# Kernel optimization log

Hardware: AMD Instinct MI355X
Metric: run time of the kernel (lower is better)

Reference implementation:

```python
import jax, jax.numpy as jnp
import numpy as np

HEADS = 2
C1 = 33    # per-head out channels, conv1
C2 = 550   # per-head out channels, conv2


def _lin_params(key, fan_in, fan_out):
    kw, kb = jax.random.split(key)
    scale = 1.0 / np.sqrt(fan_in)
    W = jax.random.uniform(kw, (fan_in, fan_out), jnp.float32, -scale, scale)
    b = jax.random.uniform(kb, (fan_out,), jnp.float32, -scale, scale)
    return W, b


def transformer_conv(x, src, dst, Wq, bq, Wk, bk, Wv, bv, Ws, bs, heads, out_ch):
    """PyG TransformerConv (concat=True, root_weight=True, beta=False)."""
    N = x.shape[0]
    q = (x @ Wq + bq).reshape(N, heads, out_ch)  # query of target node i
    k = (x @ Wk + bk).reshape(N, heads, out_ch)  # key of source node j
    v = (x @ Wv + bv).reshape(N, heads, out_ch)  # value of source node j
    # attention logits per edge: [E, H]
    alpha = jnp.einsum('ehc,ehc->eh', q[dst], k[src]) / jnp.sqrt(jnp.float32(out_ch))
    # segment softmax over incoming edges of each dst node
    m = jax.lax.stop_gradient(jax.ops.segment_max(alpha, dst, num_segments=N))  # [N,H]
    e = jnp.exp(alpha - m[dst])
    denom = jax.ops.segment_sum(e, dst, num_segments=N)  # [N,H]
    a = e / denom[dst]
    # weighted scatter-aggregate of source values: [N,H,C]
    out = jax.ops.segment_sum(a[..., None] * v[src], dst, num_segments=N)
    out = out.reshape(N, heads * out_ch)
    # root/skip connection
    out = out + x @ Ws + bs
    return out


def setup_inputs() -> dict:
    key = jax.random.key(0)
    ks = jax.random.split(key, 10)
    N, E, IN = 20000, 120000, 256
    x = jax.random.normal(ks[0], (N, IN), jnp.float32)
    edge_index = jax.random.randint(ks[1], (2, E), 0, N, jnp.int64 if jax.config.jax_enable_x64 else jnp.int32)
    d = {'x': x, 'edge_index': edge_index}
    # conv1: IN -> heads*C1
    d['Wq1'], d['bq1'] = _lin_params(ks[2], IN, HEADS * C1)
    d['Wk1'], d['bk1'] = _lin_params(ks[3], IN, HEADS * C1)
    d['Wv1'], d['bv1'] = _lin_params(ks[4], IN, HEADS * C1)
    d['Ws1'], d['bs1'] = _lin_params(ks[5], IN, HEADS * C1)
    # conv2: heads*C1 -> heads*C2
    IN2 = HEADS * C1
    d['Wq2'], d['bq2'] = _lin_params(ks[6], IN2, HEADS * C2)
    d['Wk2'], d['bk2'] = _lin_params(ks[7], IN2, HEADS * C2)
    d['Wv2'], d['bv2'] = _lin_params(ks[8], IN2, HEADS * C2)
    d['Ws2'], d['bs2'] = _lin_params(ks[9], IN2, HEADS * C2)
    return d


def reference(x, edge_index, Wq1, bq1, Wk1, bk1, Wv1, bv1, Ws1, bs1,
              Wq2, bq2, Wk2, bk2, Wv2, bv2, Ws2, bs2):
    src, dst = edge_index[0], edge_index[1]
    h = transformer_conv(x, src, dst, Wq1, bq1, Wk1, bk1, Wv1, bv1, Ws1, bs1, HEADS, C1)
    h = transformer_conv(h, src, dst, Wq2, bq2, Wk2, bk2, Wv2, bv2, Ws2, bs2, HEADS, C2)
    # x.view(N, 550, heads).max(dim=2) -- faithful to the original reshape layout
    h = h.reshape(h.shape[0], C2, HEADS)
    return jnp.max(h, axis=2)
```

## Files before the change

### kernel.cpp

```cpp
#include <hip/hip_runtime.h>
#include <math.h>

#define HEADS 2
#define C1    33
#define C2    550
#define D1    66
#define D2    1100
#define IN1   256
#define PROJW 288
#define KU    224
#define N2P   1152
#define KZ    96
#define ZW    144

typedef __attribute__((ext_vector_type(8))) short bfrag;
typedef __attribute__((ext_vector_type(4))) float f32x4;

__device__ inline unsigned short f2bf(float f) {
    unsigned int u = __float_as_uint(f);
    u += 0x7FFFu + ((u >> 16) & 1u);
    return (unsigned short)(u >> 16);
}

__device__ inline int xcd_slot(int bid, int slots) {
    return (bid >> 3) + (bid & 7) * slots;
}

__global__ void k_cvt(const float* __restrict__ x, unsigned short* __restrict__ xb, int total4) {
    int i = blockIdx.x * blockDim.x + threadIdx.x;
    if (i >= total4) return;
    float4 v = ((const float4*)x)[i];
    ushort4 o;
    o.x = f2bf(v.x); o.y = f2bf(v.y); o.z = f2bf(v.z); o.w = f2bf(v.w);
    ((ushort4*)xb)[i] = o;
}

__global__ void k_prep1(const float* __restrict__ Wq, const float* __restrict__ bq,
                        const float* __restrict__ Wk, const float* __restrict__ bk,
                        const float* __restrict__ Wv, const float* __restrict__ bv,
                        const float* __restrict__ Ws, const float* __restrict__ bs,
                        unsigned short* __restrict__ Wt1, float* __restrict__ bcat) {
    int bid = blockIdx.x;
    int lk = bid & 3, t = bid >> 2;
    int ks = t & 7, g = t >> 3;
    int col = threadIdx.x;
    int c = g * 96 + col;
    int k0 = ks * 32 + lk * 8;
    short vals[8];
    float bia = 0.f;
    if (c < 4 * D1) {
        int m = c / D1, j = c % D1;
        const float* W; const float* B;
        switch (m) {
            case 0: W = Wq; B = bq; break;
            case 1: W = Wk; B = bk; break;
            case 2: W = Wv; B = bv; break;
            default: W = Ws; B = bs; break;
        }
        #pragma unroll
        for (int e = 0; e < 8; e++) vals[e] = (short)f2bf(W[(size_t)(k0 + e) * D1 + j]);
        bia = B[j];
    } else {
        #pragma unroll
        for (int e = 0; e < 8; e++) vals[e] = 0;
    }
    *(bfrag*)&Wt1[((size_t)bid * 96 + col) * 8] = *(bfrag*)vals;
    if (ks == 0 && lk == 0) bcat[c] = bia;
}

__global__ void k_prep2(const float* __restrict__ Wv2, const float* __restrict__ bv2,
                        const float* __restrict__ Ws2, const float* __restrict__ bs2,
                        unsigned short* __restrict__ W2t) {
    int bid = blockIdx.x;
    int lk = bid & 3, t = bid >> 2;
    int ks = t % 7, g = t / 7;
    int col = threadIdx.x;
    int c = g * 96 + col;
    int k0 = ks * 32 + lk * 8;
    short vals[8];
    #pragma unroll
    for (int e = 0; e < 8; e++) {
        int k = k0 + e;
        float val = 0.f;
        if (c < D2) {
            if (c < C2) {
                if (k < 66) val = Wv2[(size_t)k * D2 + c];
                else if (k >= 132 && k < 198) val = Ws2[(size_t)(k - 132) * D2 + c];
                else if (k == 198) val = bv2[c];
                else if (k == 223) val = bs2[c];
            } else {
                if (k >= 66 && k < 132) val = Wv2[(size_t)(k - 66) * D2 + c];
                else if (k >= 132 && k < 198) val = Ws2[(size_t)(k - 132) * D2 + c];
                else if (k == 199) val = bv2[c];
                else if (k == 223) val = bs2[c];
            }
        }
        vals[e] = (short)f2bf(val);
    }
    *(bfrag*)&W2t[((size_t)bid * 96 + col) * 8] = *(bfrag*)vals;
}

__global__ void k_hist(const int* __restrict__ dst, int E, int* __restrict__ cnt) {
    int e = blockIdx.x * blockDim.x + threadIdx.x;
    if (e < E) atomicAdd(&cnt[dst[e]], 1);
}

__global__ void k_scan(const int* __restrict__ cnt, int* __restrict__ roff,
                       int* __restrict__ pos, int N) {
    __shared__ int wsum[16];
    __shared__ int carry_s;
    int tid = threadIdx.x, wid = tid >> 6, lane = tid & 63;
    if (tid == 0) { carry_s = 0; roff[0] = 0; }
    __syncthreads();
    for (int base = 0; base < N; base += 1024) {
        int i = base + tid;
        int v = (i < N) ? cnt[i] : 0;
        int x = v;
        #pragma unroll
        for (int s = 1; s < 64; s <<= 1) {
            int t = __shfl_up(x, s, 64);
            if (lane >= s) x += t;
        }
        if (lane == 63) wsum[wid] = x;
        __syncthreads();
        if (tid < 16) {
            int y = wsum[tid];
            #pragma unroll
            for (int s = 1; s < 16; s <<= 1) {
                int t = __shfl_up(y, s, 16);
                if (tid >= s) y += t;
            }
            wsum[tid] = y;
        }
        __syncthreads();
        int carry = carry_s;
        int incl = carry + (wid ? wsum[wid - 1] : 0) + x;
        if (i < N) { roff[i + 1] = incl; pos[i] = incl - v; }
        __syncthreads();
        if (tid == 0) carry_s = carry + wsum[15];
        __syncthreads();
    }
}

__global__ void k_fill(const int* __restrict__ src, const int* __restrict__ dst, int E,
                       int* __restrict__ pos, int* __restrict__ elist) {
    int e = blockIdx.x * blockDim.x + threadIdx.x;
    if (e < E) {
        int slot = atomicAdd(&pos[dst[e]], 1);
        elist[slot] = src[e];
    }
}

__global__ __launch_bounds__(256) void k_mm1(
        const unsigned short* __restrict__ A, const unsigned short* __restrict__ B,
        const float* __restrict__ bias, float* __restrict__ proj, int N,
        int nRow, int slots) {
    int s = xcd_slot(blockIdx.x, slots);
    if (s >= nRow * 3) return;
    int rowt = s / 3, g = s - rowt * 3;
    int cbase = g * 96;
    int wave = threadIdx.x >> 6, lane = threadIdx.x & 63;
    int lr = lane & 15, lk = lane >> 4;
    int rbase = rowt * 128 + wave * 32;
    int ar[2];
    #pragma unroll
    for (int mi = 0; mi < 2; mi++) {
        int r = rbase + mi * 16 + lr;
        ar[mi] = (r < N) ? r : (N - 1);
    }
    bfrag a[2][8];
    #pragma unroll
    for (int mi = 0; mi < 2; mi++)
        #pragma unroll
        for (int ks = 0; ks < 8; ks++)
            a[mi][ks] = *(const bfrag*)(A + (size_t)ar[mi] * IN1 + ks * 32 + lk * 8);
    f32x4 acc[2][6];
    #pragma unroll
    for (int mi = 0; mi < 2; mi++)
        #pragma unroll
        for (int ni = 0; ni < 6; ni++) acc[mi][ni] = (f32x4){0.f, 0.f, 0.f, 0.f};
    #pragma unroll
    for (int ks = 0; ks < 8; ks++) {
        bfrag b[6];
        #pragma unroll
        for (int ni = 0; ni < 6; ni++)
            b[ni] = *(const bfrag*)(B + (size_t)(g * 8 + ks) * 3072 + lk * 768 + (ni * 16 + lr) * 8);
        #pragma unroll
        for (int mi = 0; mi < 2; mi++)
            #pragma unroll
            for (int ni = 0; ni < 6; ni++)
                acc[mi][ni] = __builtin_amdgcn_mfma_f32_16x16x32_bf16(a[mi][ks], b[ni], acc[mi][ni], 0, 0, 0);
    }
    #pragma unroll
    for (int mi = 0; mi < 2; mi++) {
        #pragma unroll
        for (int ni = 0; ni < 6; ni++) {
            int col = cbase + ni * 16 + lr;
            float bia = bias[col];
            #pragma unroll
            for (int r = 0; r < 4; r++) {
                int row = rbase + mi * 16 + lk * 4 + r;
                if (row < N) proj[(size_t)row * PROJW + col] = acc[mi][ni][r] + bia;
            }
        }
    }
}

__global__ __launch_bounds__(128) void k_conv1(
        const float* __restrict__ proj, const int* __restrict__ roff,
        const int* __restrict__ elist, float* __restrict__ h1,
        unsigned short* __restrict__ h1b, int N) {
    int n = blockIdx.x;
    int h = threadIdx.x >> 6;
    int lane = threadIdx.x & 63;
    size_t pb = (size_t)n * PROJW;
    int hc = h * C1;
    bool ok = (lane < C1);
    float my_q = ok ? proj[pb + hc + lane] : 0.f;
    float s1v  = ok ? proj[pb + 198 + hc + lane] : 0.f;
    float m = -INFINITY, lsum = 0.f, acc = 0.f;
    int e0 = roff[n], e1 = roff[n + 1];
    const float isc = 0.17407765595569785f;
    int e = e0;
    for (; e + 3 < e1; e += 4) {
        int s0 = elist[e], s1 = elist[e + 1], s2 = elist[e + 2], s3 = elist[e + 3];
        size_t b0 = (size_t)s0 * PROJW, b1 = (size_t)s1 * PROJW;
        size_t b2 = (size_t)s2 * PROJW, b3 = (size_t)s3 * PROJW;
        float k0 = ok ? proj[b0 + 66 + hc + lane] : 0.f;
        float k1 = ok ? proj[b1 + 66 + hc + lane] : 0.f;
        float k2 = ok ? proj[b2 + 66 + hc + lane] : 0.f;
        float k3 = ok ? proj[b3 + 66 + hc + lane] : 0.f;
        float v0 = ok ? proj[b0 + 132 + hc + lane] : 0.f;
        float v1 = ok ? proj[b1 + 132 + hc + lane] : 0.f;
        float v2 = ok ? proj[b2 + 132 + hc + lane] : 0.f;
        float v3 = ok ? proj[b3 + 132 + hc + lane] : 0.f;
        float p0 = my_q * k0, p1 = my_q * k1, p2 = my_q * k2, p3 = my_q * k3;
        #pragma unroll
        for (int off = 32; off >= 1; off >>= 1) {
            p0 += __shfl_xor(p0, off, 64);
            p1 += __shfl_xor(p1, off, 64);
            p2 += __shfl_xor(p2, off, 64);
            p3 += __shfl_xor(p3, off, 64);
        }
        float a0 = p0 * isc, a1 = p1 * isc, a2 = p2 * isc, a3 = p3 * isc;
        float mp = fmaxf(fmaxf(a0, a1), fmaxf(a2, a3));
        float e0v = __expf(a0 - mp), e1v = __expf(a1 - mp);
        float e2v = __expf(a2 - mp), e3v = __expf(a3 - mp);
        float lp = (e0v + e1v) + (e2v + e3v);
        float ap = (e0v * v0 + e1v * v1) + (e2v * v2 + e3v * v3);
        float mnew = fmaxf(m, mp);
        float sc = __expf(m - mnew), sp = __expf(mp - mnew);
        lsum = lsum * sc + lp * sp;
        acc  = acc * sc + ap * sp;
        m = mnew;
    }
    for (; e + 1 < e1; e += 2) {
        int sa = elist[e], sb = elist[e + 1];
        size_t ba = (size_t)sa * PROJW, bb = (size_t)sb * PROJW;
        float ka = ok ? proj[ba + 66 + hc + lane] : 0.f;
        float va = ok ? proj[ba + 132 + hc + lane] : 0.f;
        float kb = ok ? proj[bb + 66 + hc + lane] : 0.f;
        float vb = ok ? proj[bb + 132 + hc + lane] : 0.f;
        float pa = my_q * ka, pbv = my_q * kb;
        #pragma unroll
        for (int off = 32; off >= 1; off >>= 1) {
            pa  += __shfl_xor(pa, off, 64);
            pbv += __shfl_xor(pbv, off, 64);
        }
        float aa = pa * isc, ab = pbv * isc;
        float mp = fmaxf(aa, ab);
        float ea = __expf(aa - mp), eb = __expf(ab - mp);
        float lp = ea + eb, ap = ea * va + eb * vb;
        float mnew = fmaxf(m, mp);
        float sc = __expf(m - mnew), sp = __expf(mp - mnew);
        lsum = lsum * sc + lp * sp;
        acc  = acc * sc + ap * sp;
        m = mnew;
    }
    if (e < e1) {
        int s = elist[e];
        size_t sb = (size_t)s * PROJW;
        float kv = ok ? proj[sb + 66 + hc + lane] : 0.f;
        float vv = ok ? proj[sb + 132 + hc + lane] : 0.f;
        float prod = my_q * kv;
        #pragma unroll
        for (int off = 32; off >= 1; off >>= 1) prod += __shfl_xor(prod, off, 64);
        float alpha = prod * isc;
        float mnew = fmaxf(m, alpha);
        float sc = __expf(m - mnew);
        float p = __expf(alpha - mnew);
        lsum = lsum * sc + p;
        acc  = acc * sc + p * vv;
        m = mnew;
    }
    if (ok) {
        float res = (lsum > 0.f) ? acc / lsum : 0.f;
        float val = res + s1v;
        h1[(size_t)n * D1 + hc + lane] = val;
        h1b[(size_t)n * KZ + hc + lane] = f2bf(val);
    } else if (h == 1 && lane >= C1 && lane < C1 + 30) {
        h1b[(size_t)n * KZ + D1 + (lane - C1)] = 0;
    }
}

__global__ __launch_bounds__(256) void k_precomp(
        const float* __restrict__ Wq2, const float* __restrict__ bq2,
        const float* __restrict__ Wk2, const float* __restrict__ bk2,
        float* __restrict__ G, float* __restrict__ wqbk,
        float* __restrict__ wkbq, float* __restrict__ cc) {
    int wave = threadIdx.x >> 6, lane = threadIdx.x & 63;
    int j = blockIdx.x * 4 + wave;
    if (j >= 8978) return;
    const float *u, *v;
    float* outp;
    if (j < 8976) {
        int h = j / 4488;
        int r = j % 4488;
        int a = r / 68, b = r % 68;
        if (b < 66)      { u = Wq2 + (size_t)a * D2 + h * C2; v = Wk2 + (size_t)b * D2 + h * C2; outp = &G[h * 4356 + a * 66 + b]; }
        else if (b == 66){ u = Wq2 + (size_t)a * D2 + h * C2; v = bk2 + h * C2;                  outp = &wqbk[h * 66 + a]; }
        else             { u = Wk2 + (size_t)a * D2 + h * C2; v = bq2 + h * C2;                  outp = &wkbq[h * 66 + a]; }
    } else {
        int h = j - 8976;
        u = bq2 + h * C2; v = bk2 + h * C2; outp = &cc[h];
    }
    float acc = 0.f;
    for (int c = lane; c < C2; c += 64) acc += u[c] * v[c];
    #pragma unroll
    for (int off = 32; off >= 1; off >>= 1) acc += __shfl_xor(acc, off, 64);
    if (lane == 0) *outp = acc;
}

__global__ void k_prepz(const float* __restrict__ G, const float* __restrict__ wqbk,
                        const float* __restrict__ wkbq, unsigned short* __restrict__ GBt) {
    int bid = blockIdx.x;
    int lk = bid & 3, t = bid >> 2;
    int ks = t % 3, g = t / 3;
    int col = threadIdx.x;
    int r = g * 96 + col;
    int k0 = ks * 32 + lk * 8;
    short vals[8];
    #pragma unroll
    for (int e = 0; e < 8; e++) {
        int k = k0 + e;
        float v = 0.f;
        if (k < D1) {
            if (r < 132) v = G[r * D1 + k];
            else if (r < 134) v = wqbk[(r - 132) * D1 + k];
            else if (r < 136) v = wkbq[(r - 134) * D1 + k];
        }
        vals[e] = (short)f2bf(v);
    }
    *(bfrag*)&GBt[((size_t)bid * 96 + col) * 8] = *(bfrag*)vals;
}

__global__ __launch_bounds__(256) void k_mmz(
        const unsigned short* __restrict__ A, const unsigned short* __restrict__ B,
        float* __restrict__ Z, int N, int nRow, int slots) {
    int s = xcd_slot(blockIdx.x, slots);
    if (s >= nRow * 2) return;
    int rowt = s >> 1, g = s & 1;
    int wave = threadIdx.x >> 6, lane = threadIdx.x & 63;
    int lr = lane & 15, lk = lane >> 4;
    int rbase = rowt * 64 + (wave >> 1) * 32;
    int ch = (wave & 1) * 48;
    int cbase = g * 96 + ch;
    f32x4 acc[2][3];
    #pragma unroll
    for (int i = 0; i < 2; i++)
        #pragma unroll
        for (int j = 0; j < 3; j++) acc[i][j] = (f32x4){0.f, 0.f, 0.f, 0.f};
    int ar[2];
    #pragma unroll
    for (int mi = 0; mi < 2; mi++) {
        int r = rbase + mi * 16 + lr;
        ar[mi] = (r < N) ? r : (N - 1);
    }
    #pragma unroll
    for (int ks = 0; ks < 3; ks++) {
        bfrag a[2], b[3];
        #pragma unroll
        for (int mi = 0; mi < 2; mi++)
            a[mi] = *(const bfrag*)(A + (size_t)ar[mi] * KZ + ks * 32 + lk * 8);
        #pragma unroll
        for (int ni = 0; ni < 3; ni++)
            b[ni] = *(const bfrag*)(B + (size_t)(g * 3 + ks) * 3072 + lk * 768 + (ch + ni * 16 + lr) * 8);
        #pragma unroll
        for (int mi = 0; mi < 2; mi++)
            #pragma unroll
            for (int ni = 0; ni < 3; ni++)
                acc[mi][ni] = __builtin_amdgcn_mfma_f32_16x16x32_bf16(a[mi], b[ni], acc[mi][ni], 0, 0, 0);
    }
    #pragma unroll
    for (int mi = 0; mi < 2; mi++) {
        #pragma unroll
        for (int ni = 0; ni < 3; ni++) {
            int col = cbase + ni * 16 + lr;
            if (col >= 136) continue;
            #pragma unroll
            for (int r = 0; r < 4; r++) {
                int row = rbase + mi * 16 + lk * 4 + r;
                if (row < N) Z[(size_t)row * ZW + col] = acc[mi][ni][r];
            }
        }
    }
}

__global__ __launch_bounds__(128) void k_conv2(
        const float* __restrict__ h1, const float* __restrict__ Z,
        const float* __restrict__ cc, const int* __restrict__ roff,
        const int* __restrict__ elist, unsigned short* __restrict__ U, int N) {
    int n = blockIdx.x;
    int h = threadIdx.x >> 6;
    int lane = threadIdx.x & 63;
    int c0 = lane, c1 = lane + 64;
    bool ok1 = (c1 < D1);
    float hd0 = h1[(size_t)n * D1 + c0];
    float hd1 = ok1 ? h1[(size_t)n * D1 + c1] : 0.f;
    float adv = Z[(size_t)n * ZW + 132 + h] + cc[h];
    float m = -INFINITY, lsum = 0.f, a0 = 0.f, a1 = 0.f;
    int e0 = roff[n], e1 = roff[n + 1];
    const float isc = 0.04264014327112209f;
    int hD = h * D1;
    int e = e0;
    for (; e + 3 < e1; e += 4) {
        int s0 = elist[e], s1 = elist[e + 1], s2 = elist[e + 2], s3 = elist[e + 3];
        const float* z0 = Z + (size_t)s0 * ZW;
        const float* z1 = Z + (size_t)s1 * ZW;
        const float* z2 = Z + (size_t)s2 * ZW;
        const float* z3 = Z + (size_t)s3 * ZW;
        float p0 = hd0 * z0[hD + c0] + (ok1 ? hd1 * z0[hD + c1] : 0.f);
        float p1 = hd0 * z1[hD + c0] + (ok1 ? hd1 * z1[hD + c1] : 0.f);
        float p2 = hd0 * z2[hD + c0] + (ok1 ? hd1 * z2[hD + c1] : 0.f);
        float p3 = hd0 * z3[hD + c0] + (ok1 ? hd1 * z3[hD + c1] : 0.f);
        #pragma unroll
        for (int off = 32; off >= 1; off >>= 1) {
            p0 += __shfl_xor(p0, off, 64);
            p1 += __shfl_xor(p1, off, 64);
            p2 += __shfl_xor(p2, off, 64);
            p3 += __shfl_xor(p3, off, 64);
        }
        float al0 = (p0 + adv + z0[134 + h]) * isc;
        float al1 = (p1 + adv + z1[134 + h]) * isc;
        float al2 = (p2 + adv + z2[134 + h]) * isc;
        float al3 = (p3 + adv + z3[134 + h]) * isc;
        float va00 = h1[(size_t)s0 * D1 + c0];
        float va01 = ok1 ? h1[(size_t)s0 * D1 + c1] : 0.f;
        float va10 = h1[(size_t)s1 * D1 + c0];
        float va11 = ok1 ? h1[(size_t)s1 * D1 + c1] : 0.f;
        float va20 = h1[(size_t)s2 * D1 + c0];
        float va21 = ok1 ? h1[(size_t)s2 * D1 + c1] : 0.f;
        float va30 = h1[(size_t)s3 * D1 + c0];
        float va31 = ok1 ? h1[(size_t)s3 * D1 + c1] : 0.f;
        float mp = fmaxf(fmaxf(al0, al1), fmaxf(al2, al3));
        float e0v = __expf(al0 - mp), e1v = __expf(al1 - mp);
        float e2v = __expf(al2 - mp), e3v = __expf(al3 - mp);
        float lp = (e0v + e1v) + (e2v + e3v);
        float ap0 = (e0v * va00 + e1v * va10) + (e2v * va20 + e3v * va30);
        float ap1 = (e0v * va01 + e1v * va11) + (e2v * va21 + e3v * va31);
        float mnew = fmaxf(m, mp);
        float sc = __expf(m - mnew), sp = __expf(mp - mnew);
        lsum = lsum * sc + lp * sp;
        a0 = a0 * sc + ap0 * sp;
        a1 = a1 * sc + ap1 * sp;
        m = mnew;
    }
    for (; e + 1 < e1; e += 2) {
        int sa = elist[e], sb = elist[e + 1];
        const float* za = Z + (size_t)sa * ZW;
        const float* zb = Z + (size_t)sb * ZW;
        float pa = hd0 * za[hD + c0] + (ok1 ? hd1 * za[hD + c1] : 0.f);
        float pb = hd0 * zb[hD + c0] + (ok1 ? hd1 * zb[hD + c1] : 0.f);
        #pragma unroll
        for (int off = 32; off >= 1; off >>= 1) {
            pa += __shfl_xor(pa, off, 64);
            pb += __shfl_xor(pb, off, 64);
        }
        float aa = (pa + adv + za[134 + h]) * isc;
        float ab = (pb + adv + zb[134 + h]) * isc;
        float va0 = h1[(size_t)sa * D1 + c0];
        float va1 = ok1 ? h1[(size_t)sa * D1 + c1] : 0.f;
        float vb0 = h1[(size_t)sb * D1 + c0];
        float vb1 = ok1 ? h1[(size_t)sb * D1 + c1] : 0.f;
        float mp = fmaxf(aa, ab);
        float ea = __expf(aa - mp), eb = __expf(ab - mp);
        float lp = ea + eb;
        float ap0 = ea * va0 + eb * vb0;
        float ap1 = ea * va1 + eb * vb1;
        float mnew = fmaxf(m, mp);
        float sc = __expf(m - mnew), sp = __expf(mp - mnew);
        lsum = lsum * sc + lp * sp;
        a0 = a0 * sc + ap0 * sp;
        a1 = a1 * sc + ap1 * sp;
        m = mnew;
    }
    if (e < e1) {
        int s = elist[e];
        const float* zr = Z + (size_t)s * ZW;
        float prod = hd0 * zr[hD + c0] + (ok1 ? hd1 * zr[hD + c1] : 0.f);
        #pragma unroll
        for (int off = 32; off >= 1; off >>= 1) prod += __shfl_xor(prod, off, 64);
        float alpha = (prod + adv + zr[134 + h]) * isc;
        float mnew = fmaxf(m, alpha);
        float sc = __expf(m - mnew);
        float p = __expf(alpha - mnew);
        lsum = lsum * sc + p;
        float v0 = h1[(size_t)s * D1 + c0];
        float vv1 = ok1 ? h1[(size_t)s * D1 + c1] : 0.f;
        a0 = a0 * sc + p * v0;
        a1 = a1 * sc + p * vv1;
        m = mnew;
    }
    float inv = (lsum > 0.f) ? 1.f / lsum : 0.f;
    size_t ub = (size_t)n * KU;
    U[ub + hD + c0] = f2bf(a0 * inv);
    if (ok1) U[ub + hD + c1] = f2bf(a1 * inv);
    if (lane == 0) U[ub + 198 + h] = (lsum > 0.f) ? (unsigned short)0x3F80 : (unsigned short)0;
    if (h == 0) {
        U[ub + 132 + c0] = f2bf(hd0);
        if (ok1) U[ub + 132 + c1] = f2bf(hd1);
        if (lane == 1) U[ub + 223] = (unsigned short)0x3F80;
    } else if (lane >= 34 && lane < 57) {
        U[ub + 200 + (lane - 34)] = 0;
    }
}

__global__ __launch_bounds__(256) void k_mm2(
        const unsigned short* __restrict__ A, const unsigned short* __restrict__ B,
        float* __restrict__ out, int N, int nRow, int slots) {
    __shared__ float ot[4][32][49];
    int s = xcd_slot(blockIdx.x, slots);
    if (s >= nRow * 12) return;
    int rowt = s / 12, g = s - rowt * 12;
    int wave = threadIdx.x >> 6, lane = threadIdx.x & 63;
    int lr = lane & 15, lk = lane >> 4;
    int rbase = rowt * 128 + wave * 32;
    int ar[2];
    #pragma unroll
    for (int mi = 0; mi < 2; mi++) {
        int r = rbase + mi * 16 + lr;
        ar[mi] = (r < N) ? r : (N - 1);
    }
    bfrag a[2][7];
    #pragma unroll
    for (int mi = 0; mi < 2; mi++)
        #pragma unroll
        for (int ks = 0; ks < 7; ks++)
            a[mi][ks] = *(const bfrag*)(A + (size_t)ar[mi] * KU + ks * 32 + lk * 8);
    f32x4 acc[2][6];
    #pragma unroll
    for (int mi = 0; mi < 2; mi++)
        #pragma unroll
        for (int ni = 0; ni < 6; ni++) acc[mi][ni] = (f32x4){0.f, 0.f, 0.f, 0.f};
    #pragma unroll
    for (int ks = 0; ks < 7; ks++) {
        bfrag b[6];
        #pragma unroll
        for (int ni = 0; ni < 6; ni++)
            b[ni] = *(const bfrag*)(B + (size_t)(g * 7 + ks) * 3072 + lk * 768 + (ni * 16 + lr) * 8);
        #pragma unroll
        for (int mi = 0; mi < 2; mi++)
            #pragma unroll
            for (int ni = 0; ni < 6; ni++)
                acc[mi][ni] = __builtin_amdgcn_mfma_f32_16x16x32_bf16(a[mi][ks], b[ni], acc[mi][ni], 0, 0, 0);
    }
    #pragma unroll
    for (int mi = 0; mi < 2; mi++) {
        #pragma unroll
        for (int ni = 0; ni < 6; ni++) {
            #pragma unroll
            for (int r = 0; r < 4; r++) {
                float val = acc[mi][ni][r];
                float oth = __shfl_xor(val, 1, 64);
                if (!(lane & 1))
                    ot[wave][mi * 16 + lk * 4 + r][ni * 8 + (lr >> 1)] = fmaxf(val, oth);
            }
        }
    }
    __syncthreads();
    int colb = g * 48;
    #pragma unroll
    for (int i = 0; i < 24; i++) {
        int t = i * 64 + lane;
        int r32 = t / 48, pos = t - r32 * 48;
        int row = rbase + r32;
        int col = colb + pos;
        if (row < N && col < C2)
            out[(size_t)row * C2 + col] = ot[wave][r32][pos];
    }
}

extern "C" void kernel_launch(void* const* d_in, const int* in_sizes, int n_in,
                              void* d_out, int out_size, void* d_ws, size_t ws_size,
                              hipStream_t stream) {
    const float* x  = (const float*)d_in[0];
    const int*   ei = (const int*)d_in[1];
    int N = in_sizes[0] / IN1;
    int E = in_sizes[1] / 2;
    const int* src = ei;
    const int* dst = ei + E;

    const float *Wq1 = (const float*)d_in[2],  *bq1 = (const float*)d_in[3];
    const float *Wk1 = (const float*)d_in[4],  *bk1 = (const float*)d_in[5];
    const float *Wv1 = (const float*)d_in[6],  *bv1 = (const float*)d_in[7];
    const float *Ws1 = (const float*)d_in[8],  *bs1 = (const float*)d_in[9];
    const float *Wq2 = (const float*)d_in[10], *bq2 = (const float*)d_in[11];
    const float *Wk2 = (const float*)d_in[12], *bk2 = (const float*)d_in[13];
    const float *Wv2 = (const float*)d_in[14], *bv2 = (const float*)d_in[15];
    const float *Ws2 = (const float*)d_in[16], *bs2 = (const float*)d_in[17];

    char* w = (char*)d_ws;
    size_t off = 0;
    auto take = [&](size_t bytes) { size_t o = off; off = (off + bytes + 255) & ~(size_t)255; return o; };

    unsigned short* xb = (unsigned short*)(w + take((size_t)N * IN1 * 2));
    size_t proj_off = take((size_t)N * PROJW * 4);
    float* proj = (float*)(w + proj_off);
    float* Z = proj;
    unsigned short* U = (unsigned short*)(w + proj_off + (size_t)N * ZW * 4);
    float* h1   = (float*)(w + take((size_t)N * D1 * 4));
    unsigned short* h1b = (unsigned short*)(w + take((size_t)N * KZ * 2));
    float* G    = (float*)(w + take((size_t)2 * D1 * D1 * 4));
    float* wqbk = (float*)(w + take(2 * D1 * 4));
    float* wkbq = (float*)(w + take(2 * D1 * 4));
    float* cc   = (float*)(w + take(2 * 4));
    unsigned short* GBt = (unsigned short*)(w + take((size_t)24 * 96 * 8 * 2));
    unsigned short* Wt1 = (unsigned short*)(w + take((size_t)96 * 96 * 8 * 2));
    float* bcat = (float*)(w + take(PROJW * 4));
    unsigned short* W2t = (unsigned short*)(w + take((size_t)336 * 96 * 8 * 2));
    int* cnt   = (int*)(w + take((size_t)N * 4));
    int* roff  = (int*)(w + take((size_t)(N + 1) * 4));
    int* pos   = (int*)(w + take((size_t)N * 4));
    int* elist = (int*)(w + take((size_t)E * 4));

    hipMemsetAsync(cnt, 0, (size_t)N * sizeof(int), stream);
    k_hist<<<(E + 255) / 256, 256, 0, stream>>>(dst, E, cnt);
    k_scan<<<1, 1024, 0, stream>>>(cnt, roff, pos, N);
    k_fill<<<(E + 255) / 256, 256, 0, stream>>>(src, dst, E, pos, elist);

    k_cvt<<<(N * IN1 / 4 + 255) / 256, 256, 0, stream>>>(x, xb, N * IN1 / 4);
    k_prep1<<<96, 96, 0, stream>>>(Wq1, bq1, Wk1, bk1, Wv1, bv1, Ws1, bs1, Wt1, bcat);
    k_prep2<<<336, 96, 0, stream>>>(Wv2, bv2, Ws2, bs2, W2t);
    k_precomp<<<(8978 + 3) / 4, 256, 0, stream>>>(Wq2, bq2, Wk2, bk2, G, wqbk, wkbq, cc);
    k_prepz<<<24, 96, 0, stream>>>(G, wqbk, wkbq, GBt);

    int nRow1 = (N + 127) / 128;
    int tot1  = nRow1 * 3;
    int slots1 = (tot1 + 7) / 8;
    int nRowZ = (N + 63) / 64;
    int totZ  = nRowZ * 2;
    int slotsZ = (totZ + 7) / 8;
    int nRow2 = (N + 127) / 128;
    int tot2  = nRow2 * 12;
    int slots2 = (tot2 + 7) / 8;

    k_mm1<<<slots1 * 8, 256, 0, stream>>>(xb, Wt1, bcat, proj, N, nRow1, slots1);
    k_conv1<<<N, 128, 0, stream>>>(proj, roff, elist, h1, h1b, N);

    k_mmz<<<slotsZ * 8, 256, 0, stream>>>(h1b, GBt, Z, N, nRowZ, slotsZ);

    k_conv2<<<N, 128, 0, stream>>>(h1, Z, cc, roff, elist, U, N);

    k_mm2<<<slots2 * 8, 256, 0, stream>>>(U, W2t, (float*)d_out, N, nRow2, slots2);
}
```

Measured before the change: 174.8 us.

## Split each wave into two half-waves processing alternate edges in graph attention kernels

Both edge-aggregation kernels (conv1 and conv2) now give each 32-lane half of a wavefront alternating edges. Each half handles its feature slice with 32-wide lane coverage and reduces dot products with 5-step 32-lane shuffles instead of 6-step 64-lane ones. At the end the two halves' online-softmax partial states (max, sum, accumulators) are merged with cross-half shuffles. This is meant to use idle lanes (33 of 64 were active in conv1) and to halve per-edge shuffle latency. In exchange it adds a few extra predicated loads and a final merge step.

```diff
diff --git a/kernel.cpp b/kernel.cpp
--- a/kernel.cpp
+++ b/kernel.cpp
@@ -213,93 +213,89 @@
     int n = blockIdx.x;
     int h = threadIdx.x >> 6;
     int lane = threadIdx.x & 63;
+    int half = lane >> 5, l32 = lane & 31;
     size_t pb = (size_t)n * PROJW;
     int hc = h * C1;
-    bool ok = (lane < C1);
-    float my_q = ok ? proj[pb + hc + lane] : 0.f;
-    float s1v  = ok ? proj[pb + 198 + hc + lane] : 0.f;
-    float m = -INFINITY, lsum = 0.f, acc = 0.f;
-    int e0 = roff[n], e1 = roff[n + 1];
+    float q_a = proj[pb + hc + l32];
+    float q_b = (l32 == 0) ? proj[pb + hc + 32] : 0.f;
+    int E0 = roff[n], E1 = roff[n + 1];
+    float m = -INFINITY, lsum = 0.f, aca = 0.f, acb = 0.f;
     const float isc = 0.17407765595569785f;
-    int e = e0;
-    for (; e + 3 < e1; e += 4) {
-        int s0 = elist[e], s1 = elist[e + 1], s2 = elist[e + 2], s3 = elist[e + 3];
+    int i = E0 + half;
+    for (; i + 2 < E1; i += 4) {
+        int s0 = elist[i], s1 = elist[i + 2];
         size_t b0 = (size_t)s0 * PROJW, b1 = (size_t)s1 * PROJW;
-        size_t b2 = (size_t)s2 * PROJW, b3 = (size_t)s3 * PROJW;
-        float k0 = ok ? proj[b0 + 66 + hc + lane] : 0.f;
-        float k1 = ok ? proj[b1 + 66 + hc + lane] : 0.f;
-        float k2 = ok ? proj[b2 + 66 + hc + lane] : 0.f;
-        float k3 = ok ? proj[b3 + 66 + hc + lane] : 0.f;
-        float v0 = ok ? proj[b0 + 132 + hc + lane] : 0.f;
-        float v1 = ok ? proj[b1 + 132 + hc + lane] : 0.f;
-        float v2 = ok ? proj[b2 + 132 + hc + lane] : 0.f;
-        float v3 = ok ? proj[b3 + 132 + hc + lane] : 0.f;
-        float p0 = my_q * k0, p1 = my_q * k1, p2 = my_q * k2, p3 = my_q * k3;
-        #pragma unroll
-        for (int off = 32; off >= 1; off >>= 1) {
-            p0 += __shfl_xor(p0, off, 64);
-            p1 += __shfl_xor(p1, off, 64);
-            p2 += __shfl_xor(p2, off, 64);
-            p3 += __shfl_xor(p3, off, 64);
-        }
-        float a0 = p0 * isc, a1 = p1 * isc, a2 = p2 * isc, a3 = p3 * isc;
-        float mp = fmaxf(fmaxf(a0, a1), fmaxf(a2, a3));
-        float e0v = __expf(a0 - mp), e1v = __expf(a1 - mp);
-        float e2v = __expf(a2 - mp), e3v = __expf(a3 - mp);
-        float lp = (e0v + e1v) + (e2v + e3v);
-        float ap = (e0v * v0 + e1v * v1) + (e2v * v2 + e3v * v3);
+        float k0a = proj[b0 + 66 + hc + l32];
+        float k0b = (l32 == 0) ? proj[b0 + 66 + hc + 32] : 0.f;
+        float k1a = proj[b1 + 66 + hc + l32];
+        float k1b = (l32 == 0) ? proj[b1 + 66 + hc + 32] : 0.f;
+        float v0a = proj[b0 + 132 + hc + l32];
+        float v0b = (l32 == 0) ? proj[b0 + 132 + hc + 32] : 0.f;
+        float v1a = proj[b1 + 132 + hc + l32];
+        float v1b = (l32 == 0) ? proj[b1 + 132 + hc + 32] : 0.f;
+        float p0 = q_a * k0a + q_b * k0b;
+        float p1 = q_a * k1a + q_b * k1b;
+        #pragma unroll
+        for (int off = 16; off >= 1; off >>= 1) {
+            p0 += __shfl_xor(p0, off, 32);
+            p1 += __shfl_xor(p1, off, 32);
+        }
+        float a0 = p0 * isc, a1 = p1 * isc;
+        float mp = fmaxf(a0, a1);
+        float e0 = __expf(a0 - mp), e1 = __expf(a1 - mp);
+        float lp = e0 + e1;
+        float apa = e0 * v0a + e1 * v1a;
+        float apb = e0 * v0b + e1 * v1b;
         float mnew = fmaxf(m, mp);
         float sc = __expf(m - mnew), sp = __expf(mp - mnew);
         lsum = lsum * sc + lp * sp;
-        acc  = acc * sc + ap * sp;
+        aca = aca * sc + apa * sp;
+        acb = acb * sc + apb * sp;
         m = mnew;
     }
-    for (; e + 1 < e1; e += 2) {
-        int sa = elist[e], sb = elist[e + 1];
-        size_t ba = (size_t)sa * PROJW, bb = (size_t)sb * PROJW;
-        float ka = ok ? proj[ba + 66 + hc + lane] : 0.f;
-        float va = ok ? proj[ba + 132 + hc + lane] : 0.f;
-        float kb = ok ? proj[bb + 66 + hc + lane] : 0.f;
-        float vb = ok ? proj[bb + 132 + hc + lane] : 0.f;
-        float pa = my_q * ka, pbv = my_q * kb;
-        #pragma unroll
-        for (int off = 32; off >= 1; off >>= 1) {
-            pa  += __shfl_xor(pa, off, 64);
-            pbv += __shfl_xor(pbv, off, 64);
-        }
-        float aa = pa * isc, ab = pbv * isc;
-        float mp = fmaxf(aa, ab);
-        float ea = __expf(aa - mp), eb = __expf(ab - mp);
-        float lp = ea + eb, ap = ea * va + eb * vb;
-        float mnew = fmaxf(m, mp);
-        float sc = __expf(m - mnew), sp = __expf(mp - mnew);
-        lsum = lsum * sc + lp * sp;
-        acc  = acc * sc + ap * sp;
-        m = mnew;
-    }
-    if (e < e1) {
-        int s = elist[e];
+    for (; i < E1; i += 2) {
+        int s = elist[i];
         size_t sb = (size_t)s * PROJW;
-        float kv = ok ? proj[sb + 66 + hc + lane] : 0.f;
-        float vv = ok ? proj[sb + 132 + hc + lane] : 0.f;
-        float prod = my_q * kv;
-        #pragma unroll
-        for (int off = 32; off >= 1; off >>= 1) prod += __shfl_xor(prod, off, 64);
-        float alpha = prod * isc;
+        float ka = proj[sb + 66 + hc + l32];
+        float kb = (l32 == 0) ? proj[sb + 66 + hc + 32] : 0.f;
+        float va = proj[sb + 132 + hc + l32];
+        float vb = (l32 == 0) ? proj[sb + 132 + hc + 32] : 0.f;
+        float p = q_a * ka + q_b * kb;
+        #pragma unroll
+        for (int off = 16; off >= 1; off >>= 1) p += __shfl_xor(p, off, 32);
+        float alpha = p * isc;
         float mnew = fmaxf(m, alpha);
         float sc = __expf(m - mnew);
-        float p = __expf(alpha - mnew);
-        lsum = lsum * sc + p;
-        acc  = acc * sc + p * vv;
+        float pe = __expf(alpha - mnew);
+        lsum = lsum * sc + pe;
+        aca = aca * sc + pe * va;
+        acb = acb * sc + pe * vb;
         m = mnew;
     }
-    if (ok) {
-        float res = (lsum > 0.f) ? acc / lsum : 0.f;
-        float val = res + s1v;
-        h1[(size_t)n * D1 + hc + lane] = val;
-        h1b[(size_t)n * KZ + hc + lane] = f2bf(val);
-    } else if (h == 1 && lane >= C1 && lane < C1 + 30) {
-        h1b[(size_t)n * KZ + D1 + (lane - C1)] = 0;
+    float mO  = __shfl_xor(m, 32, 64);
+    float lO  = __shfl_xor(lsum, 32, 64);
+    float aaO = __shfl_xor(aca, 32, 64);
+    float abO = __shfl_xor(acb, 32, 64);
+    float mnew = fmaxf(m, mO);
+    float sS = (m  > -INFINITY) ? __expf(m  - mnew) : 0.f;
+    float sO = (mO > -INFINITY) ? __expf(mO - mnew) : 0.f;
+    lsum = lsum * sS + lO * sO;
+    aca  = aca * sS + aaO * sO;
+    acb  = acb * sS + abO * sO;
+    float inv = (lsum > 0.f) ? 1.f / lsum : 0.f;
+    if (half == 0) {
+        float s1a = proj[pb + 198 + hc + l32];
+        float val = aca * inv + s1a;
+        h1[(size_t)n * D1 + hc + l32] = val;
+        h1b[(size_t)n * KZ + hc + l32] = f2bf(val);
+        if (l32 == 0) {
+            float s1b = proj[pb + 198 + hc + 32];
+            float valb = acb * inv + s1b;
+            h1[(size_t)n * D1 + hc + 32] = valb;
+            h1b[(size_t)n * KZ + hc + 32] = f2bf(valb);
+        }
+    } else if (h == 1 && l32 < 30) {
+        h1b[(size_t)n * KZ + D1 + l32] = 0;
     }
 }
 
@@ -413,115 +409,101 @@
     int n = blockIdx.x;
     int h = threadIdx.x >> 6;
     int lane = threadIdx.x & 63;
-    int c0 = lane, c1 = lane + 64;
-    bool ok1 = (c1 < D1);
-    float hd0 = h1[(size_t)n * D1 + c0];
-    float hd1 = ok1 ? h1[(size_t)n * D1 + c1] : 0.f;
+    int half = lane >> 5, l32 = lane & 31;
+    int hD = h * D1;
+    size_t nb = (size_t)n * D1;
+    float hd_a = h1[nb + l32];
+    float hd_b = h1[nb + 32 + l32];
+    float hd_c = (l32 < 2) ? h1[nb + 64 + l32] : 0.f;
     float adv = Z[(size_t)n * ZW + 132 + h] + cc[h];
-    float m = -INFINITY, lsum = 0.f, a0 = 0.f, a1 = 0.f;
-    int e0 = roff[n], e1 = roff[n + 1];
+    int E0 = roff[n], E1 = roff[n + 1];
+    float m = -INFINITY, lsum = 0.f, aa = 0.f, ab = 0.f, ac = 0.f;
     const float isc = 0.04264014327112209f;
-    int hD = h * D1;
-    int e = e0;
-    for (; e + 3 < e1; e += 4) {
-        int s0 = elist[e], s1 = elist[e + 1], s2 = elist[e + 2], s3 = elist[e + 3];
+    int i = E0 + half;
+    for (; i + 2 < E1; i += 4) {
+        int s0 = elist[i], s1 = elist[i + 2];
         const float* z0 = Z + (size_t)s0 * ZW;
         const float* z1 = Z + (size_t)s1 * ZW;
-        const float* z2 = Z + (size_t)s2 * ZW;
-        const float* z3 = Z + (size_t)s3 * ZW;
-        float p0 = hd0 * z0[hD + c0] + (ok1 ? hd1 * z0[hD + c1] : 0.f);
-        float p1 = hd0 * z1[hD + c0] + (ok1 ? hd1 * z1[hD + c1] : 0.f);
-        float p2 = hd0 * z2[hD + c0] + (ok1 ? hd1 * z2[hD + c1] : 0.f);
-        float p3 = hd0 * z3[hD + c0] + (ok1 ? hd1 * z3[hD + c1] : 0.f);
-        #pragma unroll
-        for (int off = 32; off >= 1; off >>= 1) {
-            p0 += __shfl_xor(p0, off, 64);
-            p1 += __shfl_xor(p1, off, 64);
-            p2 += __shfl_xor(p2, off, 64);
-            p3 += __shfl_xor(p3, off, 64);
-        }
-        float al0 = (p0 + adv + z0[134 + h]) * isc;
-        float al1 = (p1 + adv + z1[134 + h]) * isc;
-        float al2 = (p2 + adv + z2[134 + h]) * isc;
-        float al3 = (p3 + adv + z3[134 + h]) * isc;
-        float va00 = h1[(size_t)s0 * D1 + c0];
-        float va01 = ok1 ? h1[(size_t)s0 * D1 + c1] : 0.f;
-        float va10 = h1[(size_t)s1 * D1 + c0];
-        float va11 = ok1 ? h1[(size_t)s1 * D1 + c1] : 0.f;
-        float va20 = h1[(size_t)s2 * D1 + c0];
-        float va21 = ok1 ? h1[(size_t)s2 * D1 + c1] : 0.f;
-        float va30 = h1[(size_t)s3 * D1 + c0];
-        float va31 = ok1 ? h1[(size_t)s3 * D1 + c1] : 0.f;
-        float mp = fmaxf(fmaxf(al0, al1), fmaxf(al2, al3));
-        float e0v = __expf(al0 - mp), e1v = __expf(al1 - mp);
-        float e2v = __expf(al2 - mp), e3v = __expf(al3 - mp);
-        float lp = (e0v + e1v) + (e2v + e3v);
-        float ap0 = (e0v * va00 + e1v * va10) + (e2v * va20 + e3v * va30);
-        float ap1 = (e0v * va01 + e1v * va11) + (e2v * va21 + e3v * va31);
+        float z0c = (l32 < 2) ? z0[hD + 64 + l32] : 0.f;
+        float z1c = (l32 < 2) ? z1[hD + 64 + l32] : 0.f;
+        float p0 = hd_a * z0[hD + l32] + hd_b * z0[hD + 32 + l32] + hd_c * z0c;
+        float p1 = hd_a * z1[hD + l32] + hd_b * z1[hD + 32 + l32] + hd_c * z1c;
+        float as0 = z0[134 + h], as1 = z1[134 + h];
+        #pragma unroll
+        for (int off = 16; off >= 1; off >>= 1) {
+            p0 += __shfl_xor(p0, off, 32);
+            p1 += __shfl_xor(p1, off, 32);
+        }
+        float al0 = (p0 + adv + as0) * isc;
+        float al1 = (p1 + adv + as1) * isc;
+        size_t v0b = (size_t)s0 * D1, v1b = (size_t)s1 * D1;
+        float v0a = h1[v0b + l32], v0bb = h1[v0b + 32 + l32];
+        float v0c = (l32 < 2) ? h1[v0b + 64 + l32] : 0.f;
+        float v1a = h1[v1b + l32], v1bb = h1[v1b + 32 + l32];
+        float v1c = (l32 < 2) ? h1[v1b + 64 + l32] : 0.f;
+        float mp = fmaxf(al0, al1);
+        float e0 = __expf(al0 - mp), e1 = __expf(al1 - mp);
+        float lp = e0 + e1;
         float mnew = fmaxf(m, mp);
         float sc = __expf(m - mnew), sp = __expf(mp - mnew);
         lsum = lsum * sc + lp * sp;
-        a0 = a0 * sc + ap0 * sp;
-        a1 = a1 * sc + ap1 * sp;
+        aa = aa * sc + (e0 * v0a + e1 * v1a) * sp;
+        ab = ab * sc + (e0 * v0bb + e1 * v1bb) * sp;
+        ac = ac * sc + (e0 * v0c + e1 * v1c) * sp;
         m = mnew;
     }
-    for (; e + 1 < e1; e += 2) {
-        int sa = elist[e], sb = elist[e + 1];
-        const float* za = Z + (size_t)sa * ZW;
-        const float* zb = Z + (size_t)sb * ZW;
-        float pa = hd0 * za[hD + c0] + (ok1 ? hd1 * za[hD + c1] : 0.f);
-        float pb = hd0 * zb[hD + c0] + (ok1 ? hd1 * zb[hD + c1] : 0.f);
-        #pragma unroll
-        for (int off = 32; off >= 1; off >>= 1) {
-            pa += __shfl_xor(pa, off, 64);
-            pb += __shfl_xor(pb, off, 64);
-        }
-        float aa = (pa + adv + za[134 + h]) * isc;
-        float ab = (pb + adv + zb[134 + h]) * isc;
-        float va0 = h1[(size_t)sa * D1 + c0];
-        float va1 = ok1 ? h1[(size_t)sa * D1 + c1] : 0.f;
-        float vb0 = h1[(size_t)sb * D1 + c0];
-        float vb1 = ok1 ? h1[(size_t)sb * D1 + c1] : 0.f;
-        float mp = fmaxf(aa, ab);
-        float ea = __expf(aa - mp), eb = __expf(ab - mp);
-        float lp = ea + eb;
-        float ap0 = ea * va0 + eb * vb0;
-        float ap1 = ea * va1 + eb * vb1;
-        float mnew = fmaxf(m, mp);
-        float sc = __expf(m - mnew), sp = __expf(mp - mnew);
-        lsum = lsum * sc + lp * sp;
-        a0 = a0 * sc + ap0 * sp;
-        a1 = a1 * sc + ap1 * sp;
-        m = mnew;
-    }
-    if (e < e1) {
-        int s = elist[e];
+    for (; i < E1; i += 2) {
+        int s = elist[i];
         const float* zr = Z + (size_t)s * ZW;
-        float prod = hd0 * zr[hD + c0] + (ok1 ? hd1 * zr[hD + c1] : 0.f);
-        #pragma unroll
-        for (int off = 32; off >= 1; off >>= 1) prod += __shfl_xor(prod, off, 64);
-        float alpha = (prod + adv + zr[134 + h]) * isc;
+        float zc = (l32 < 2) ? zr[hD + 64 + l32] : 0.f;
+        float p = hd_a * zr[hD + l32] + hd_b * zr[hD + 32 + l32] + hd_c * zc;
+        float as_ = zr[134 + h];
+        #pragma unroll
+        for (int off = 16; off >= 1; off >>= 1) p += __shfl_xor(p, off, 32);
+        float alpha = (p + adv + as_) * isc;
+        size_t vb = (size_t)s * D1;
+        float va = h1[vb + l32], vbb = h1[vb + 32 + l32];
+        float vc = (l32 < 2) ? h1[vb + 64 + l32] : 0.f;
         float mnew = fmaxf(m, alpha);
         float sc = __expf(m - mnew);
-        float p = __expf(alpha - mnew);
-        lsum = lsum * sc + p;
-        float v0 = h1[(size_t)s * D1 + c0];
-        float vv1 = ok1 ? h1[(size_t)s * D1 + c1] : 0.f;
-        a0 = a0 * sc + p * v0;
-        a1 = a1 * sc + p * vv1;
+        float pe = __expf(alpha - mnew);
+        lsum = lsum * sc + pe;
+        aa = aa * sc + pe * va;
+        ab = ab * sc + pe * vbb;
+        ac = ac * sc + pe * vc;
         m = mnew;
     }
+    float mO  = __shfl_xor(m, 32, 64);
+    float lO  = __shfl_xor(lsum, 32, 64);
+    float aaO = __shfl_xor(aa, 32, 64);
+    float abO = __shfl_xor(ab, 32, 64);
+    float acO = __shfl_xor(ac, 32, 64);
+    float mnew = fmaxf(m, mO);
+    float sS = (m  > -INFINITY) ? __expf(m  - mnew) : 0.f;
+    float sO = (mO > -INFINITY) ? __expf(mO - mnew) : 0.f;
+    lsum = lsum * sS + lO * sO;
+    aa = aa * sS + aaO * sO;
+    ab = ab * sS + abO * sO;
+    ac = ac * sS + acO * sO;
     float inv = (lsum > 0.f) ? 1.f / lsum : 0.f;
     size_t ub = (size_t)n * KU;
-    U[ub + hD + c0] = f2bf(a0 * inv);
-    if (ok1) U[ub + hD + c1] = f2bf(a1 * inv);
+    if (half == 0) {
+        U[ub + hD + l32] = f2bf(aa * inv);
+        if (l32 < 2) U[ub + hD + 64 + l32] = f2bf(ac * inv);
+    } else {
+        U[ub + hD + 32 + l32] = f2bf(ab * inv);
+    }
     if (lane == 0) U[ub + 198 + h] = (lsum > 0.f) ? (unsigned short)0x3F80 : (unsigned short)0;
     if (h == 0) {
-        U[ub + 132 + c0] = f2bf(hd0);
-        if (ok1) U[ub + 132 + c1] = f2bf(hd1);
-        if (lane == 1) U[ub + 223] = (unsigned short)0x3F80;
-    } else if (lane >= 34 && lane < 57) {
-        U[ub + 200 + (lane - 34)] = 0;
+        if (half == 0) {
+            U[ub + 132 + l32] = f2bf(hd_a);
+            if (l32 < 2) U[ub + 132 + 64 + l32] = f2bf(hd_c);
+            if (l32 == 2) U[ub + 223] = (unsigned short)0x3F80;
+        } else {
+            U[ub + 132 + 32 + l32] = f2bf(hd_b);
+        }
+    } else if (half == 1 && l32 < 23) {
+        U[ub + 200 + l32] = 0;
     }
 }
 
```

After: 173.1 us. Within noise of the previous version (-1.0%).
